# Optimization experiments

Hardware: AMD Instinct MI355X
Metric: run time of the kernel (lower is better)

Reference implementation:

```python
import jax, jax.numpy as jnp
import numpy as np

N_TYPES = 7
DT = 0.1
TAU_INIT = 20.0


def setup_inputs() -> dict:
    key = jax.random.key(0)
    k0, k1, k2, k3 = jax.random.split(key, 4)
    N = 49000          # n_neurons, divisible by 7 types
    E = 1_600_000      # n_edges (~avg degree 32)
    B = 8              # batch (via explicit v_init)
    n_tm1 = N // N_TYPES
    type_ids = (jnp.arange(N) % N_TYPES).astype(jnp.int32)   # type 0 == 'Tm1'
    tm1_indices = jnp.arange(0, N, N_TYPES, dtype=jnp.int32)  # positions where type_ids==0
    return {
        "tm1_input": jax.random.normal(k0, (B, n_tm1), jnp.float32),
        "v_init": jnp.zeros((B, N), jnp.float32),
        "weights": jax.random.normal(k1, (E,), jnp.float32),
        "bias": jnp.zeros((N,), jnp.float32),
        "tau_params": jnp.full((N_TYPES,), TAU_INIT, jnp.float32),
        "scale_excitatory": jnp.ones((), jnp.float32),
        "scale_inhibitory": jnp.ones((), jnp.float32),
        "source_indices": jax.random.randint(k2, (E,), 0, N, dtype=jnp.int32),
        "target_indices": jax.random.randint(k3, (E,), 0, N, dtype=jnp.int32),
        "type_ids": type_ids,
        "tm1_indices": tm1_indices,
        "steps": 100,
    }


def reference(tm1_input, v_init, weights, bias, tau_params,
              scale_excitatory, scale_inhibitory,
              source_indices, target_indices, type_ids, tm1_indices, steps):
    # per-neuron tau from per-type params (torch: get_tau_vector via masks)
    tau = tau_params[type_ids]                                   # [N]
    one = jnp.ones((), weights.dtype)
    edge_scales = jnp.where(weights > 0, scale_excitatory,
                            jnp.where(weights < 0, scale_inhibitory, one))
    scaled_weights = weights * edge_scales                       # [E]

    def step(v, _):
        v = v.at[:, tm1_indices].set(tm1_input)                  # clamp Tm1 neurons
        r = jax.nn.relu(v)                                       # activation
        edge_currents = r[:, source_indices] * scaled_weights    # gather [B,E]
        syn = jnp.zeros_like(v).at[:, target_indices].add(edge_currents)  # scatter-add [B,N]
        dv = (-v + syn + bias) / tau
        dv = dv.at[:, tm1_indices].set(0.0)                      # Tm1 held fixed
        return v + DT * dv, None

    v, _ = jax.lax.scan(step, v_init, None, length=steps)
    return v
```

## Files before the change

kernel.cpp:

```cpp
#include <hip/hip_runtime.h>


#define BLK 256
#define STEPS 100
#define NBATCH 8
#define PRE 6
static constexpr float DT_C = 0.1f;

__device__ __forceinline__ unsigned f2bf_rne(float x) {
    unsigned u = __float_as_uint(x);
    return (u + 0x7FFFu + ((u >> 16) & 1u)) >> 16;
}
__device__ __forceinline__ unsigned pk_bf2(float a, float b) {
    return f2bf_rne(a) | (f2bf_rne(b) << 16);
}

__global__ void k_zero(int* counts, int* tm1_pos, int N) {
    int i = blockIdx.x * BLK + threadIdx.x;
    if (i < N) { counts[i] = 0; tm1_pos[i] = -1; }
}

__global__ void k_tm1pos(const int* __restrict__ tm1_idx, int* tm1_pos, int NT) {
    int i = blockIdx.x * BLK + threadIdx.x;
    if (i < NT) tm1_pos[tm1_idx[i]] = i;
}

__global__ void k_hist(const int* __restrict__ tgt, int* counts, int E) {
    int i = blockIdx.x * BLK + threadIdx.x;
    if (i < E) atomicAdd(&counts[tgt[i]], 1);
}

__global__ void k_scan1(const int* __restrict__ counts, int* offsets, int* bsum, int N) {
    __shared__ int s[BLK];
    int tx = threadIdx.x;
    int i = blockIdx.x * BLK + tx;
    int v = (i < N) ? counts[i] : 0;
    s[tx] = v; __syncthreads();
    for (int d = 1; d < BLK; d <<= 1) {
        int t = (tx >= d) ? s[tx - d] : 0;
        __syncthreads();
        s[tx] += t;
        __syncthreads();
    }
    if (i < N) offsets[i] = s[tx] - v;
    if (tx == BLK - 1) bsum[blockIdx.x] = s[tx];
}

__global__ void k_scan2(int* bsum, int nb) {
    __shared__ int s[BLK];
    int tx = threadIdx.x;
    int v = (tx < nb) ? bsum[tx] : 0;
    s[tx] = v; __syncthreads();
    for (int d = 1; d < BLK; d <<= 1) {
        int t = (tx >= d) ? s[tx - d] : 0;
        __syncthreads();
        s[tx] += t;
        __syncthreads();
    }
    if (tx < nb) bsum[tx] = s[tx] - v;
}

__global__ void k_scan3(const int* __restrict__ bsum, int* offsets, int* cursor, int N, int E) {
    int i = blockIdx.x * BLK + threadIdx.x;
    if (i < N) {
        int o = offsets[i] + bsum[i >> 8];
        offsets[i] = o;
        cursor[i] = o;
    } else if (i == N) {
        offsets[N] = E;
    }
}

__global__ void k_fill(const int* __restrict__ srcI, const int* __restrict__ tgtI,
                       const float* __restrict__ w,
                       const float* __restrict__ se, const float* __restrict__ si,
                       int* cursor, unsigned* __restrict__ csr, int E) {
    int i = blockIdx.x * BLK + threadIdx.x;
    if (i >= E) return;
    float wv = w[i];
    float sc = wv > 0.f ? se[0] : (wv < 0.f ? si[0] : 1.f);
    float sw = wv * sc;
    unsigned entry = (f2bf_rne(sw) << 16) | (unsigned)srcI[i];
    int t = tgtI[i];
    int pos = atomicAdd(&cursor[t], 1);
    csr[pos] = entry;
}

__global__ void k_initv(const float* __restrict__ tm1_in, const float* __restrict__ v_init,
                        const float* __restrict__ bias, const float* __restrict__ tau_p,
                        const int* __restrict__ type_ids, const int* __restrict__ tm1_pos,
                        float* __restrict__ v_w, uint4* __restrict__ r0, uint4* __restrict__ r1,
                        float4* __restrict__ coef, int N, int NT) {
    int n = blockIdx.x * BLK + threadIdx.x;
    if (n >= N) return;
    int k = tm1_pos[n];
    float tau = tau_p[type_ids[n]];
    float g = DT_C / tau;
    coef[n] = make_float4(1.f - g, g, bias[n] * g, (k >= 0) ? 1.f : 0.f);
    float vv[NBATCH], rr[NBATCH];
    for (int b = 0; b < NBATCH; ++b) {
        float val = (k >= 0) ? tm1_in[b * NT + k] : v_init[b * N + n];
        vv[b] = val;
        rr[b] = fmaxf(val, 0.f);
    }
    float4* vp = (float4*)(v_w + (size_t)n * 8);
    vp[0] = make_float4(vv[0], vv[1], vv[2], vv[3]);
    vp[1] = make_float4(vv[4], vv[5], vv[6], vv[7]);
    uint4 rq = make_uint4(pk_bf2(rr[0], rr[1]), pk_bf2(rr[2], rr[3]),
                          pk_bf2(rr[4], rr[5]), pk_bf2(rr[6], rr[7]));
    r0[n] = rq;
    r1[n] = rq;
}

__device__ __forceinline__ float butterfly8(float4 a0, float4 a1, int sub) {
    int bit0 = sub & 1, bit1 = (sub >> 1) & 1, bit2 = (sub >> 2) & 1;
    float b0 = (bit0 ? a0.y : a0.x) + __shfl_xor(bit0 ? a0.x : a0.y, 1);
    float b1 = (bit0 ? a0.w : a0.z) + __shfl_xor(bit0 ? a0.z : a0.w, 1);
    float b2 = (bit0 ? a1.y : a1.x) + __shfl_xor(bit0 ? a1.x : a1.y, 1);
    float b3 = (bit0 ? a1.w : a1.z) + __shfl_xor(bit0 ? a1.z : a1.w, 1);
    float c0 = (bit1 ? b1 : b0) + __shfl_xor(bit1 ? b0 : b1, 2);
    float c1 = (bit1 ? b3 : b2) + __shfl_xor(bit1 ? b2 : b3, 2);
    return (bit2 ? c1 : c0) + __shfl_xor(bit2 ? c0 : c1, 4);
}

__global__ __launch_bounds__(BLK) void k_step(
        const int* __restrict__ offsets, const unsigned* __restrict__ csr,
        const float4* __restrict__ coef, const uint4* __restrict__ r_prev,
        float* __restrict__ v_w, unsigned short* __restrict__ r_next, int N) {
    int tid = blockIdx.x * BLK + threadIdx.x;
    int n = tid >> 3;
    int sub = threadIdx.x & 7;
    if (n >= N) return;
    float4 cf = coef[n];
    if (cf.w != 0.f) return;
    int s = offsets[n], e = offsets[n + 1];

    float wj[PRE];
    int   sj[PRE];
    #pragma unroll
    for (int j = 0; j < PRE; ++j) {
        int idx = s + sub + 8 * j;
        unsigned ew = (idx < e) ? csr[idx] : 0u;
        wj[j] = __uint_as_float(ew & 0xFFFF0000u);
        sj[j] = (int)(ew & 0xFFFFu);
    }
    uint4 q[PRE];
    #pragma unroll
    for (int j = 0; j < PRE; ++j) {
        int idx = s + sub + 8 * j;
        q[j] = (idx < e) ? r_prev[sj[j]] : make_uint4(0u, 0u, 0u, 0u);
    }
    float4 a0 = make_float4(0.f, 0.f, 0.f, 0.f);
    float4 a1 = make_float4(0.f, 0.f, 0.f, 0.f);
    #pragma unroll
    for (int j = 0; j < PRE; ++j) {
        float w = wj[j];
        a0.x = fmaf(w, __uint_as_float(q[j].x << 16),          a0.x);
        a0.y = fmaf(w, __uint_as_float(q[j].x & 0xFFFF0000u),  a0.y);
        a0.z = fmaf(w, __uint_as_float(q[j].y << 16),          a0.z);
        a0.w = fmaf(w, __uint_as_float(q[j].y & 0xFFFF0000u),  a0.w);
        a1.x = fmaf(w, __uint_as_float(q[j].z << 16),          a1.x);
        a1.y = fmaf(w, __uint_as_float(q[j].z & 0xFFFF0000u),  a1.y);
        a1.z = fmaf(w, __uint_as_float(q[j].w << 16),          a1.z);
        a1.w = fmaf(w, __uint_as_float(q[j].w & 0xFFFF0000u),  a1.w);
    }
    for (int i = s + sub + 8 * PRE; i < e; i += 8) {
        unsigned ew = csr[i];
        float w = __uint_as_float(ew & 0xFFFF0000u);
        uint4 qq = r_prev[ew & 0xFFFFu];
        a0.x = fmaf(w, __uint_as_float(qq.x << 16),          a0.x);
        a0.y = fmaf(w, __uint_as_float(qq.x & 0xFFFF0000u),  a0.y);
        a0.z = fmaf(w, __uint_as_float(qq.y << 16),          a0.z);
        a0.w = fmaf(w, __uint_as_float(qq.y & 0xFFFF0000u),  a0.w);
        a1.x = fmaf(w, __uint_as_float(qq.z << 16),          a1.x);
        a1.y = fmaf(w, __uint_as_float(qq.z & 0xFFFF0000u),  a1.y);
        a1.z = fmaf(w, __uint_as_float(qq.w << 16),          a1.z);
        a1.w = fmaf(w, __uint_as_float(qq.w & 0xFFFF0000u),  a1.w);
    }
    float syn = butterfly8(a0, a1, sub);
    size_t idx = (size_t)n * 8 + sub;
    float vo = v_w[idx];
    float vn = vo * cf.x + syn * cf.y + cf.z;
    v_w[idx] = vn;
    r_next[idx] = (unsigned short)f2bf_rne(fmaxf(vn, 0.f));
}

__global__ void k_out(const float* __restrict__ v_w, float* __restrict__ out, int N) {
    int t = blockIdx.x * BLK + threadIdx.x;
    if (t >= NBATCH * N) return;
    int b = t / N;
    int n = t - b * N;
    out[t] = v_w[(size_t)n * 8 + b];
}

static inline size_t align16(size_t x) { return (x + 15) & ~(size_t)15; }

extern "C" void kernel_launch(void* const* d_in, const int* in_sizes, int n_in,
                              void* d_out, int out_size, void* d_ws, size_t ws_size,
                              hipStream_t stream) {
    const float* tm1_in  = (const float*)d_in[0];
    const float* v_init  = (const float*)d_in[1];
    const float* weights = (const float*)d_in[2];
    const float* bias    = (const float*)d_in[3];
    const float* tau_p   = (const float*)d_in[4];
    const float* se      = (const float*)d_in[5];
    const float* si      = (const float*)d_in[6];
    const int*   srcI    = (const int*)d_in[7];
    const int*   tgtI    = (const int*)d_in[8];
    const int*   type_ids= (const int*)d_in[9];
    const int*   tm1_idx = (const int*)d_in[10];

    const int E  = in_sizes[2];
    const int N  = in_sizes[3];
    const int NT = in_sizes[10];

    char* p = (char*)d_ws;
    size_t off = 0;
    auto take = [&](size_t bytes) { void* r = p + off; off += align16(bytes); return r; };
    int*      offsets = (int*)     take((size_t)(N + 1) * 4);
    int*      cursor  = (int*)     take((size_t)N * 4);
    int*      counts  = (int*)     take((size_t)N * 4);
    int*      tm1_pos = (int*)     take((size_t)N * 4);
    int*      bsum    = (int*)     take(1024 * 4);
    unsigned* csr     = (unsigned*)take((size_t)E * 4);
    float4*   coef    = (float4*)  take((size_t)N * 16);
    float*    v_w     = (float*)   take((size_t)N * 8 * 4);
    uint4*    r0      = (uint4*)   take((size_t)N * 16);
    uint4*    r1      = (uint4*)   take((size_t)N * 16);
    (void)ws_size;

    const int gN  = (N + BLK - 1) / BLK;
    const int gN1 = (N + 1 + BLK - 1) / BLK;
    const int gE  = (E + BLK - 1) / BLK;
    const int gNT = (NT + BLK - 1) / BLK;
    const int gS  = (N * NBATCH + BLK - 1) / BLK;

    k_zero<<<gN, BLK, 0, stream>>>(counts, tm1_pos, N);
    k_tm1pos<<<gNT, BLK, 0, stream>>>(tm1_idx, tm1_pos, NT);
    k_hist<<<gE, BLK, 0, stream>>>(tgtI, counts, E);
    k_scan1<<<gN, BLK, 0, stream>>>(counts, offsets, bsum, N);
    k_scan2<<<1, BLK, 0, stream>>>(bsum, gN);
    k_scan3<<<gN1, BLK, 0, stream>>>(bsum, offsets, cursor, N, E);
    k_fill<<<gE, BLK, 0, stream>>>(srcI, tgtI, weights, se, si, cursor, csr, E);
    k_initv<<<gN, BLK, 0, stream>>>(tm1_in, v_init, bias, tau_p, type_ids, tm1_pos,
                                    v_w, r0, r1, coef, N, NT);

    uint4* rb[2] = { r0, r1 };
    for (int s = 0; s < STEPS; ++s) {
        k_step<<<gS, BLK, 0, stream>>>(offsets, csr, coef, rb[s & 1],
                                       v_w, (unsigned short*)rb[(s + 1) & 1], N);
    }
    k_out<<<gS, BLK, 0, stream>>>(v_w, (float*)d_out, N);
}
```

Before: 1.210 ms.

## Precompute constant Tm1-source synaptic input once and widen per-neuron thread groups

Edges whose source is a clamped Tm1 neuron contribute a constant current every step, so each CSR row is partitioned into dynamic and static segments. A one-time k_static kernel sums the static part, folded with bias and dt/tau, into a per-neuron constant. The per-step kernel then gathers only the dynamic edges and uses 16 threads per neuron with a shorter prefetch. This drops about a seventh of per-step gather traffic, at the cost of extra setup kernels and more workspace.

```diff
diff --git a/kernel.cpp b/kernel.cpp
--- a/kernel.cpp
+++ b/kernel.cpp
@@ -4,7 +4,7 @@
 #define BLK 256
 #define STEPS 100
 #define NBATCH 8
-#define PRE 6
+#define PRE2 2
 static constexpr float DT_C = 0.1f;
 
 __device__ __forceinline__ unsigned f2bf_rne(float x) {
@@ -15,9 +15,9 @@
     return f2bf_rne(a) | (f2bf_rne(b) << 16);
 }
 
-__global__ void k_zero(int* counts, int* tm1_pos, int N) {
-    int i = blockIdx.x * BLK + threadIdx.x;
-    if (i < N) { counts[i] = 0; tm1_pos[i] = -1; }
+__global__ void k_zero(int* counts, int* countS, int* tm1_pos, int N) {
+    int i = blockIdx.x * BLK + threadIdx.x;
+    if (i < N) { counts[i] = 0; countS[i] = 0; tm1_pos[i] = -1; }
 }
 
 __global__ void k_tm1pos(const int* __restrict__ tm1_idx, int* tm1_pos, int NT) {
@@ -25,9 +25,17 @@
     if (i < NT) tm1_pos[tm1_idx[i]] = i;
 }
 
-__global__ void k_hist(const int* __restrict__ tgt, int* counts, int E) {
-    int i = blockIdx.x * BLK + threadIdx.x;
-    if (i < E) atomicAdd(&counts[tgt[i]], 1);
+__global__ void k_hist(const int* __restrict__ srcI, const int* __restrict__ tgt,
+                       const int* __restrict__ type_ids,
+                       int* counts, int* countS, unsigned char* __restrict__ flagA,
+                       int E) {
+    int i = blockIdx.x * BLK + threadIdx.x;
+    if (i >= E) return;
+    int t = tgt[i];
+    atomicAdd(&counts[t], 1);
+    unsigned char st = (type_ids[srcI[i]] == 0) ? 1 : 0;
+    if (st) atomicAdd(&countS[t], 1);
+    flagA[i] = st;
 }
 
 __global__ void k_scan1(const int* __restrict__ counts, int* offsets, int* bsum, int N) {
@@ -60,21 +68,31 @@
     if (tx < nb) bsum[tx] = s[tx] - v;
 }
 
-__global__ void k_scan3(const int* __restrict__ bsum, int* offsets, int* cursor, int N, int E) {
+__global__ void k_scan3(const int* __restrict__ bsum, int* offsets, int N, int E) {
     int i = blockIdx.x * BLK + threadIdx.x;
     if (i < N) {
-        int o = offsets[i] + bsum[i >> 8];
-        offsets[i] = o;
-        cursor[i] = o;
+        offsets[i] += bsum[i >> 8];
     } else if (i == N) {
         offsets[N] = E;
     }
+}
+
+__global__ void k_cursors(const int* __restrict__ offsets, const int* __restrict__ countS,
+                          int* cursorD, int* cursorS, int* dynEnd, int N) {
+    int i = blockIdx.x * BLK + threadIdx.x;
+    if (i >= N) return;
+    int o  = offsets[i];
+    int dE = offsets[i + 1] - countS[i];
+    cursorD[i] = o;
+    cursorS[i] = dE;
+    dynEnd[i]  = dE;
 }
 
 __global__ void k_fill(const int* __restrict__ srcI, const int* __restrict__ tgtI,
                        const float* __restrict__ w,
                        const float* __restrict__ se, const float* __restrict__ si,
-                       int* cursor, unsigned* __restrict__ csr, int E) {
+                       const unsigned char* __restrict__ flagA,
+                       int* cursorD, int* cursorS, unsigned* __restrict__ csr, int E) {
     int i = blockIdx.x * BLK + threadIdx.x;
     if (i >= E) return;
     float wv = w[i];
@@ -82,21 +100,20 @@
     float sw = wv * sc;
     unsigned entry = (f2bf_rne(sw) << 16) | (unsigned)srcI[i];
     int t = tgtI[i];
-    int pos = atomicAdd(&cursor[t], 1);
+    int pos = flagA[i] ? atomicAdd(&cursorS[t], 1) : atomicAdd(&cursorD[t], 1);
     csr[pos] = entry;
 }
 
 __global__ void k_initv(const float* __restrict__ tm1_in, const float* __restrict__ v_init,
-                        const float* __restrict__ bias, const float* __restrict__ tau_p,
+                        const float* __restrict__ tau_p,
                         const int* __restrict__ type_ids, const int* __restrict__ tm1_pos,
                         float* __restrict__ v_w, uint4* __restrict__ r0, uint4* __restrict__ r1,
                         float4* __restrict__ coef, int N, int NT) {
     int n = blockIdx.x * BLK + threadIdx.x;
     if (n >= N) return;
     int k = tm1_pos[n];
-    float tau = tau_p[type_ids[n]];
-    float g = DT_C / tau;
-    coef[n] = make_float4(1.f - g, g, bias[n] * g, (k >= 0) ? 1.f : 0.f);
+    float g = DT_C / tau_p[type_ids[n]];
+    coef[n] = make_float4(1.f - g, g, (k >= 0) ? 1.f : 0.f, 0.f);
     float vv[NBATCH], rr[NBATCH];
     for (int b = 0; b < NBATCH; ++b) {
         float val = (k >= 0) ? tm1_in[b * NT + k] : v_init[b * N + n];
@@ -123,37 +140,69 @@
     return (bit2 ? c1 : c0) + __shfl_xor(bit2 ? c0 : c1, 4);
 }
 
-__global__ __launch_bounds__(BLK) void k_step(
-        const int* __restrict__ offsets, const unsigned* __restrict__ csr,
-        const float4* __restrict__ coef, const uint4* __restrict__ r_prev,
-        float* __restrict__ v_w, unsigned short* __restrict__ r_next, int N) {
+__global__ void k_static(const int* __restrict__ offsets, const int* __restrict__ dynEnd,
+                         const unsigned* __restrict__ csr, const uint4* __restrict__ r0,
+                         const float4* __restrict__ coef, const float* __restrict__ bias,
+                         float* __restrict__ cF, int N) {
     int tid = blockIdx.x * BLK + threadIdx.x;
     int n = tid >> 3;
     int sub = threadIdx.x & 7;
     if (n >= N) return;
     float4 cf = coef[n];
-    if (cf.w != 0.f) return;
-    int s = offsets[n], e = offsets[n + 1];
-
-    float wj[PRE];
-    int   sj[PRE];
+    int s = dynEnd[n], e = offsets[n + 1];
+    float4 a0 = make_float4(0.f, 0.f, 0.f, 0.f);
+    float4 a1 = make_float4(0.f, 0.f, 0.f, 0.f);
+    for (int i = s + sub; i < e; i += 8) {
+        unsigned ew = csr[i];
+        float w = __uint_as_float(ew & 0xFFFF0000u);
+        uint4 q = r0[ew & 0xFFFFu];
+        a0.x = fmaf(w, __uint_as_float(q.x << 16),          a0.x);
+        a0.y = fmaf(w, __uint_as_float(q.x & 0xFFFF0000u),  a0.y);
+        a0.z = fmaf(w, __uint_as_float(q.y << 16),          a0.z);
+        a0.w = fmaf(w, __uint_as_float(q.y & 0xFFFF0000u),  a0.w);
+        a1.x = fmaf(w, __uint_as_float(q.z << 16),          a1.x);
+        a1.y = fmaf(w, __uint_as_float(q.z & 0xFFFF0000u),  a1.y);
+        a1.z = fmaf(w, __uint_as_float(q.w << 16),          a1.z);
+        a1.w = fmaf(w, __uint_as_float(q.w & 0xFFFF0000u),  a1.w);
+    }
+    float syn = butterfly8(a0, a1, sub);
+    cF[(size_t)n * 8 + sub] = (syn + bias[n]) * cf.y;
+}
+
+__global__ __launch_bounds__(BLK, 8) void k_step(
+        const int* __restrict__ offsets, const int* __restrict__ dynEnd,
+        const unsigned* __restrict__ csr,
+        const float4* __restrict__ coef, const float* __restrict__ cF,
+        const uint4* __restrict__ r_prev,
+        float* __restrict__ v_w, unsigned short* __restrict__ r_next, int N) {
+    int tid = blockIdx.x * BLK + threadIdx.x;
+    int n = tid >> 4;
+    if (n >= N) return;
+    int s16 = threadIdx.x & 15;
+    int sub = s16 & 7;
+    float4 cf = coef[n];
+    if (cf.z != 0.f) return;
+    int s = offsets[n], e = dynEnd[n];
+
+    float wj[PRE2];
+    int   sj[PRE2];
     #pragma unroll
-    for (int j = 0; j < PRE; ++j) {
-        int idx = s + sub + 8 * j;
+    for (int j = 0; j < PRE2; ++j) {
+        int idx = s + s16 + 16 * j;
         unsigned ew = (idx < e) ? csr[idx] : 0u;
         wj[j] = __uint_as_float(ew & 0xFFFF0000u);
         sj[j] = (int)(ew & 0xFFFFu);
     }
-    uint4 q[PRE];
+    uint4 q[PRE2];
     #pragma unroll
-    for (int j = 0; j < PRE; ++j) {
-        int idx = s + sub + 8 * j;
+    for (int j = 0; j < PRE2; ++j) {
+        int idx = s + s16 + 16 * j;
         q[j] = (idx < e) ? r_prev[sj[j]] : make_uint4(0u, 0u, 0u, 0u);
     }
     float4 a0 = make_float4(0.f, 0.f, 0.f, 0.f);
     float4 a1 = make_float4(0.f, 0.f, 0.f, 0.f);
     #pragma unroll
-    for (int j = 0; j < PRE; ++j) {
+    for (int j = 0; j < PRE2; ++j) {
         float w = wj[j];
         a0.x = fmaf(w, __uint_as_float(q[j].x << 16),          a0.x);
         a0.y = fmaf(w, __uint_as_float(q[j].x & 0xFFFF0000u),  a0.y);
@@ -164,7 +213,7 @@
         a1.z = fmaf(w, __uint_as_float(q[j].w << 16),          a1.z);
         a1.w = fmaf(w, __uint_as_float(q[j].w & 0xFFFF0000u),  a1.w);
     }
-    for (int i = s + sub + 8 * PRE; i < e; i += 8) {
+    for (int i = s + s16 + 16 * PRE2; i < e; i += 16) {
         unsigned ew = csr[i];
         float w = __uint_as_float(ew & 0xFFFF0000u);
         uint4 qq = r_prev[ew & 0xFFFFu];
@@ -178,11 +227,13 @@
         a1.w = fmaf(w, __uint_as_float(qq.w & 0xFFFF0000u),  a1.w);
     }
     float syn = butterfly8(a0, a1, sub);
-    size_t idx = (size_t)n * 8 + sub;
-    float vo = v_w[idx];
-    float vn = vo * cf.x + syn * cf.y + cf.z;
-    v_w[idx] = vn;
-    r_next[idx] = (unsigned short)f2bf_rne(fmaxf(vn, 0.f));
+    syn += __shfl_xor(syn, 8);
+    if (s16 < 8) {
+        size_t idx = (size_t)n * 8 + sub;
+        float vn = v_w[idx] * cf.x + syn * cf.y + cF[idx];
+        v_w[idx] = vn;
+        r_next[idx] = (unsigned short)f2bf_rne(fmaxf(vn, 0.f));
+    }
 }
 
 __global__ void k_out(const float* __restrict__ v_w, float* __restrict__ out, int N) {
@@ -218,12 +269,17 @@
     size_t off = 0;
     auto take = [&](size_t bytes) { void* r = p + off; off += align16(bytes); return r; };
     int*      offsets = (int*)     take((size_t)(N + 1) * 4);
-    int*      cursor  = (int*)     take((size_t)N * 4);
+    int*      cursorD = (int*)     take((size_t)N * 4);
+    int*      cursorS = (int*)     take((size_t)N * 4);
     int*      counts  = (int*)     take((size_t)N * 4);
+    int*      countS  = (int*)     take((size_t)N * 4);
+    int*      dynEnd  = (int*)     take((size_t)N * 4);
     int*      tm1_pos = (int*)     take((size_t)N * 4);
     int*      bsum    = (int*)     take(1024 * 4);
+    unsigned char* flagA = (unsigned char*)take((size_t)E);
     unsigned* csr     = (unsigned*)take((size_t)E * 4);
     float4*   coef    = (float4*)  take((size_t)N * 16);
+    float*    cF      = (float*)   take((size_t)N * 8 * 4);
     float*    v_w     = (float*)   take((size_t)N * 8 * 4);
     uint4*    r0      = (uint4*)   take((size_t)N * 16);
     uint4*    r1      = (uint4*)   take((size_t)N * 16);
@@ -233,22 +289,26 @@
     const int gN1 = (N + 1 + BLK - 1) / BLK;
     const int gE  = (E + BLK - 1) / BLK;
     const int gNT = (NT + BLK - 1) / BLK;
-    const int gS  = (N * NBATCH + BLK - 1) / BLK;
-
-    k_zero<<<gN, BLK, 0, stream>>>(counts, tm1_pos, N);
+    const int g8  = (N * 8 + BLK - 1) / BLK;
+    const int g16 = (N * 16 + BLK - 1) / BLK;
+
+    k_zero<<<gN, BLK, 0, stream>>>(counts, countS, tm1_pos, N);
     k_tm1pos<<<gNT, BLK, 0, stream>>>(tm1_idx, tm1_pos, NT);
-    k_hist<<<gE, BLK, 0, stream>>>(tgtI, counts, E);
+    k_hist<<<gE, BLK, 0, stream>>>(srcI, tgtI, type_ids, counts, countS, flagA, E);
     k_scan1<<<gN, BLK, 0, stream>>>(counts, offsets, bsum, N);
     k_scan2<<<1, BLK, 0, stream>>>(bsum, gN);
-    k_scan3<<<gN1, BLK, 0, stream>>>(bsum, offsets, cursor, N, E);
-    k_fill<<<gE, BLK, 0, stream>>>(srcI, tgtI, weights, se, si, cursor, csr, E);
-    k_initv<<<gN, BLK, 0, stream>>>(tm1_in, v_init, bias, tau_p, type_ids, tm1_pos,
+    k_scan3<<<gN1, BLK, 0, stream>>>(bsum, offsets, N, E);
+    k_cursors<<<gN, BLK, 0, stream>>>(offsets, countS, cursorD, cursorS, dynEnd, N);
+    k_fill<<<gE, BLK, 0, stream>>>(srcI, tgtI, weights, se, si, flagA,
+                                   cursorD, cursorS, csr, E);
+    k_initv<<<gN, BLK, 0, stream>>>(tm1_in, v_init, tau_p, type_ids, tm1_pos,
                                     v_w, r0, r1, coef, N, NT);
+    k_static<<<g8, BLK, 0, stream>>>(offsets, dynEnd, csr, r0, coef, bias, cF, N);
 
     uint4* rb[2] = { r0, r1 };
     for (int s = 0; s < STEPS; ++s) {
-        k_step<<<gS, BLK, 0, stream>>>(offsets, csr, coef, rb[s & 1],
-                                       v_w, (unsigned short*)rb[(s + 1) & 1], N);
-    }
-    k_out<<<gS, BLK, 0, stream>>>(v_w, (float*)d_out, N);
-}
+        k_step<<<g16, BLK, 0, stream>>>(offsets, dynEnd, csr, coef, cF, rb[s & 1],
+                                        v_w, (unsigned short*)rb[(s + 1) & 1], N);
+    }
+    k_out<<<g8, BLK, 0, stream>>>(v_w, (float*)d_out, N);
+}
```

Measured after the change: 1.251 ms. +3.3%, slower.
